# Kernel optimization log

Measured on AMD Instinct MI355X. Metric: run time of the kernel, lower is better.

Reference implementation:

```python
import jax, jax.numpy as jnp
import numpy as np


def setup_inputs() -> dict:
    key = jax.random.key(0)
    k1, k2, k3, k4, k5 = jax.random.split(key, 5)
    dim, hidden = 64, 128
    x = jax.random.normal(k1, (32, 128, 128, dim), dtype=jnp.float32)
    # torch Linear stores (out,in); we store transposed so y = x @ W + b
    W_expand = jax.random.normal(k2, (dim, hidden), dtype=jnp.float32) * (1.0 / np.sqrt(dim))
    b_expand = jax.random.normal(k3, (hidden,), dtype=jnp.float32) * 0.01
    W_restore = jax.random.normal(k4, (hidden, 1), dtype=jnp.float32) * (1.0 / np.sqrt(hidden))
    b_restore = jax.random.normal(k5, (1,), dtype=jnp.float32) * 0.01
    return {
        "x": x,
        "W_expand": W_expand,
        "b_expand": b_expand,
        "W_restore": W_restore,
        "b_restore": b_restore,
        "kernel_size": 2,
        "stride": 2,
    }


def reference(x, W_expand, b_expand, W_restore, b_restore, kernel_size, stride):
    b, r, c, d = x.shape
    sr = (r - kernel_size) // stride + 1
    sc = (c - kernel_size) // stride + 1
    s = stride  # original code slices stride x stride windows
    # gather all windows at once: (b, sr, s, sc, s, d)
    ri = (jnp.arange(sr) * stride)[:, None] + jnp.arange(s)[None, :]
    ci = (jnp.arange(sc) * stride)[:, None] + jnp.arange(s)[None, :]
    win = x[:, ri[:, :, None, None], ci[None, None, :, :], :]
    # -> (b, sr, sc, s*s, d)
    win = win.transpose(0, 1, 3, 2, 4, 5).reshape(b, sr, sc, s * s, d)
    # tiny MLP attention weights per window element
    h = jnp.tanh(jnp.einsum('bqpwd,dh->bqpwh', win, W_expand) + b_expand)
    logit = jax.nn.sigmoid(jnp.einsum('bqpwh,ho->bqpwo', h, W_restore)[..., 0] + b_restore[0])
    w = jax.nn.softmax(logit, axis=-1)  # over window elements
    out = jnp.sum(win * w[..., None], axis=3)  # (b, sr, sc, d)
    return out
```

## Files before the change

kernel.cpp:

```cpp
#include <hip/hip_runtime.h>


typedef __attribute__((ext_vector_type(8))) short short8;
typedef __attribute__((ext_vector_type(4))) float floatx4;

#define B_   32
#define R_   128
#define C_   128
#define D_   64
#define H_   128
#define NW_  (B_ * 64 * 64)
#define NGRP_ (NW_ / 4)
#define NBLK_ 1024
#define NWAVE_ (NBLK_ * 4)
#define L_   (NGRP_ / NWAVE_)

#define XSTEP_ (4L * R_ * C_ * D_)
#define OSTEP_ ((long)NWAVE_ * 4 * 64)

#define L2E_  1.4426950408889634f
#define T2L_  2.8853900817779268f

__device__ __forceinline__ unsigned short f2bf_rne(float f) {
  union { float f; unsigned int u; } v; v.f = f;
  unsigned int u = v.u;
  u += 0x7fffu + ((u >> 16) & 1u);
  return (unsigned short)(u >> 16);
}

__device__ __forceinline__ unsigned int pk_bf16(float lo, float hi) {
  unsigned int a = __builtin_bit_cast(unsigned int, lo) + 0x8000u;
  unsigned int b = __builtin_bit_cast(unsigned int, hi) + 0x8000u;
  return __builtin_amdgcn_perm(b, a, 0x07060302u);
}

template <int CTRL>
__device__ __forceinline__ float dpp_add(float x) {
  int xi = __builtin_bit_cast(int, x);
  int yi = __builtin_amdgcn_update_dpp(0, xi, CTRL, 0xf, 0xf, true);
  return x + __builtin_bit_cast(float, yi);
}
#define DPP_XOR1   0xB1
#define DPP_XOR2   0x4E
#define DPP_XOR3   0x1B
#define DPP_XOR7   0x141
#define DPP_XOR15  0x140
__device__ __forceinline__ float row_reduce16(float x) {
  x = dpp_add<DPP_XOR1>(x);
  x = dpp_add<DPP_XOR3>(x);
  x = dpp_add<DPP_XOR7>(x);
  x = dpp_add<DPP_XOR15>(x);
  return x;
}
__device__ __forceinline__ float quad_sum(float x) {
  x = dpp_add<DPP_XOR1>(x);
  x = dpp_add<DPP_XOR2>(x);
  return x;
}

__global__ void prep_kernel(const float* __restrict__ We,
                            unsigned short* __restrict__ F)
{
  int t = blockIdx.x * 256 + threadIdx.x;
  int j    = t & 7;
  int lane = (t >> 3) & 63;
  int fi   = t >> 9;
  int n  = fi >> 1, ks = fi & 1;
  int quad = lane >> 4, c = lane & 15;
  F[t] = f2bf_rne(We[(ks * 32 + quad * 8 + j) * 128 + n * 16 + c]);
}

__global__ __launch_bounds__(256, 2) void softpool_kernel(
    const float* __restrict__ x, const unsigned short* __restrict__ F,
    const float* __restrict__ be, const float* __restrict__ Wr,
    const float* __restrict__ br, float* __restrict__ out)
{
  const int lane = threadIdx.x & 63;
  const int wv   = threadIdx.x >> 6;
  const int c    = lane & 15;
  const int quad = lane >> 4;

  short8 Bf[8][2];
#pragma unroll
  for (int n = 0; n < 8; ++n)
#pragma unroll
    for (int ks = 0; ks < 2; ++ks)
      Bf[n][ks] = *(const short8*)&F[((n * 2 + ks) * 64 + lane) * 8];

  float beK[8], wr2[8], swr = 0.f;
#pragma unroll
  for (int n = 0; n < 8; ++n) {
    float w = Wr[n * 16 + c];
    beK[n] = be[n * 16 + c] * T2L_;
    wr2[n] = -2.0f * w;
    swr += w;
  }
  const float brN = -L2E_ * br[0];

  const int gw = blockIdx.x * 4 + wv;

  const int w0   = gw * 4 + (c >> 2);
  const int elem = c & 3;
  const int bb = w0 >> 12;
  const int qq = (w0 >> 6) & 63;
  const int pp = w0 & 63;
  const float* xp = x + (((bb * R_ + (qq * 2 + (elem >> 1))) * C_
                          + (pp * 2 + (elem & 1))) * D_) + quad * 8;

  const int win = c >> 2;
  float* op = out + (long)(gw * 4 + win) * 64
            + quad * 8 + ((elem & 1) << 2) + ((elem & 2) << 4);

  const int  widx = (win * 16 + elem) << 2;
  const bool oddc = (c & 1) != 0;
  const bool hi2c = (c & 2) != 0;

  floatx4 st[3][4];
#pragma unroll
  for (int s = 0; s < 2; ++s) {
    const float* p = xp + (long)s * XSTEP_;
    st[s][0] = *(const floatx4*)(p);
    st[s][1] = *(const floatx4*)(p + 4);
    st[s][2] = *(const floatx4*)(p + 32);
    st[s][3] = *(const floatx4*)(p + 36);
  }

#pragma unroll
  for (int it = 0; it < L_; ++it) {
    if (it < L_ - 2) {
      const int ps = (it + 2) % 3;
      const float* p = xp + 2 * XSTEP_;
      st[ps][0] = *(const floatx4*)(p);
      st[ps][1] = *(const floatx4*)(p + 4);
      st[ps][2] = *(const floatx4*)(p + 32);
      st[ps][3] = *(const floatx4*)(p + 36);
    }

    const int cs = it % 3;
    const floatx4 a0 = st[cs][0], a1 = st[cs][1];
    const floatx4 a2 = st[cs][2], a3 = st[cs][3];

    union { unsigned int u[4]; short8 v; } A0u, A1u;
    A0u.u[0] = pk_bf16(a0[0], a0[1]); A0u.u[1] = pk_bf16(a0[2], a0[3]);
    A0u.u[2] = pk_bf16(a1[0], a1[1]); A0u.u[3] = pk_bf16(a1[2], a1[3]);
    A1u.u[0] = pk_bf16(a2[0], a2[1]); A1u.u[1] = pk_bf16(a2[2], a2[3]);
    A1u.u[2] = pk_bf16(a3[0], a3[1]); A1u.u[3] = pk_bf16(a3[2], a3[3]);

    floatx4 acc[8];
#pragma unroll
    for (int n = 0; n < 8; ++n) {
      floatx4 z = {0.f, 0.f, 0.f, 0.f};
      z = __builtin_amdgcn_mfma_f32_16x16x32_bf16(A0u.v, Bf[n][0], z, 0, 0, 0);
      acc[n] = __builtin_amdgcn_mfma_f32_16x16x32_bf16(A1u.v, Bf[n][1], z, 0, 0, 0);
    }

    float p0 = swr, p1 = swr, p2 = swr, p3 = swr;
#pragma unroll
    for (int n = 0; n < 8; ++n) {
      float e0 = __builtin_amdgcn_exp2f(fmaf(acc[n][0], T2L_, beK[n]));
      float e1 = __builtin_amdgcn_exp2f(fmaf(acc[n][1], T2L_, beK[n]));
      float e2 = __builtin_amdgcn_exp2f(fmaf(acc[n][2], T2L_, beK[n]));
      float e3 = __builtin_amdgcn_exp2f(fmaf(acc[n][3], T2L_, beK[n]));
      p0 = fmaf(wr2[n], __builtin_amdgcn_rcpf(e0 + 1.0f), p0);
      p1 = fmaf(wr2[n], __builtin_amdgcn_rcpf(e1 + 1.0f), p1);
      p2 = fmaf(wr2[n], __builtin_amdgcn_rcpf(e2 + 1.0f), p2);
      p3 = fmaf(wr2[n], __builtin_amdgcn_rcpf(e3 + 1.0f), p3);
    }
    p0 = row_reduce16(p0);
    p1 = row_reduce16(p1);
    p2 = row_reduce16(p2);
    p3 = row_reduce16(p3);
    float l0 = __builtin_amdgcn_rcpf(1.0f + __builtin_amdgcn_exp2f(fmaf(p0, -L2E_, brN)));
    float l1 = __builtin_amdgcn_rcpf(1.0f + __builtin_amdgcn_exp2f(fmaf(p1, -L2E_, brN)));
    float l2 = __builtin_amdgcn_rcpf(1.0f + __builtin_amdgcn_exp2f(fmaf(p2, -L2E_, brN)));
    float l3 = __builtin_amdgcn_rcpf(1.0f + __builtin_amdgcn_exp2f(fmaf(p3, -L2E_, brN)));
    float s0 = __builtin_amdgcn_exp2f(l0 * L2E_);
    float s1 = __builtin_amdgcn_exp2f(l1 * L2E_);
    float s2 = __builtin_amdgcn_exp2f(l2 * L2E_);
    float s3 = __builtin_amdgcn_exp2f(l3 * L2E_);
    float inv = __builtin_amdgcn_rcpf(s0 + s1 + s2 + s3);
    float w0f = s0 * inv, w1f = s1 * inv, w2f = s2 * inv, w3f = s3 * inv;

    float wa = oddc ? w1f : w0f;
    float wb = oddc ? w3f : w2f;
    float wsel = hi2c ? wb : wa;
    float W = __builtin_bit_cast(float,
        __builtin_amdgcn_ds_bpermute(widx, __builtin_bit_cast(int, wsel)));

    floatx4 t0 = a0 * W, t1 = a1 * W, t2 = a2 * W, t3 = a3 * W;
    floatx4 o0, o1, o2, o3;
#pragma unroll
    for (int j = 0; j < 4; ++j) {
      o0[j] = quad_sum(t0[j]);
      o1[j] = quad_sum(t1[j]);
      o2[j] = quad_sum(t2[j]);
      o3[j] = quad_sum(t3[j]);
    }
    floatx4 o = hi2c ? (oddc ? o3 : o2) : (oddc ? o1 : o0);
    *(floatx4*)(op) = o;

    xp += XSTEP_;
    op += OSTEP_;
  }
}

extern "C" void kernel_launch(void* const* d_in, const int* in_sizes, int n_in,
                              void* d_out, int out_size, void* d_ws, size_t ws_size,
                              hipStream_t stream) {
  const float* x  = (const float*)d_in[0];
  const float* We = (const float*)d_in[1];
  const float* be = (const float*)d_in[2];
  const float* Wr = (const float*)d_in[3];
  const float* br = (const float*)d_in[4];
  float* out = (float*)d_out;
  unsigned short* F = (unsigned short*)d_ws;

  prep_kernel<<<32, 256, 0, stream>>>(We, F);
  softpool_kernel<<<NBLK_, 256, 0, stream>>>(x, F, be, Wr, br, out);
}
```

Measured before the change: 209.5 us.

## Raise occupancy with grid-stride loop, single-stage prefetch, and more blocks

Replaces the fully unrolled 3-stage register prefetch ring with a runtime grid-stride loop that prefetches only the next iteration. Grid size goes from 1024 to 1280 blocks and launch bounds allow 5 blocks per CU instead of 2. The aim is to hide memory latency through more resident waves rather than deep per-wave buffering, which cuts register pressure. Each wave now keeps less data in flight, and the tail handling makes the last iteration issue a redundant reload.

```diff
diff --git a/kernel.cpp b/kernel.cpp
--- a/kernel.cpp
+++ b/kernel.cpp
@@ -11,12 +11,12 @@
 #define H_   128
 #define NW_  (B_ * 64 * 64)
 #define NGRP_ (NW_ / 4)
-#define NBLK_ 1024
+#define NBLK_ 1280
 #define NWAVE_ (NBLK_ * 4)
-#define L_   (NGRP_ / NWAVE_)
-
-#define XSTEP_ (4L * R_ * C_ * D_)
-#define OSTEP_ ((long)NWAVE_ * 4 * 64)
+#define GSTRIDE_ NWAVE_
+
+#define XSTEP_ (5L * R_ * C_ * D_)
+#define OSTEP_ ((long)GSTRIDE_ * 4 * 64)
 
 #define L2E_  1.4426950408889634f
 #define T2L_  2.8853900817779268f
@@ -70,7 +70,7 @@
   F[t] = f2bf_rne(We[(ks * 32 + quad * 8 + j) * 128 + n * 16 + c]);
 }
 
-__global__ __launch_bounds__(256, 2) void softpool_kernel(
+__global__ __launch_bounds__(256, 5) void softpool_kernel(
     const float* __restrict__ x, const unsigned short* __restrict__ F,
     const float* __restrict__ be, const float* __restrict__ Wr,
     const float* __restrict__ br, float* __restrict__ out)
@@ -115,30 +115,18 @@
   const bool oddc = (c & 1) != 0;
   const bool hi2c = (c & 2) != 0;
 
-  floatx4 st[3][4];
-#pragma unroll
-  for (int s = 0; s < 2; ++s) {
-    const float* p = xp + (long)s * XSTEP_;
-    st[s][0] = *(const floatx4*)(p);
-    st[s][1] = *(const floatx4*)(p + 4);
-    st[s][2] = *(const floatx4*)(p + 32);
-    st[s][3] = *(const floatx4*)(p + 36);
-  }
-
-#pragma unroll
-  for (int it = 0; it < L_; ++it) {
-    if (it < L_ - 2) {
-      const int ps = (it + 2) % 3;
-      const float* p = xp + 2 * XSTEP_;
-      st[ps][0] = *(const floatx4*)(p);
-      st[ps][1] = *(const floatx4*)(p + 4);
-      st[ps][2] = *(const floatx4*)(p + 32);
-      st[ps][3] = *(const floatx4*)(p + 36);
-    }
-
-    const int cs = it % 3;
-    const floatx4 a0 = st[cs][0], a1 = st[cs][1];
-    const floatx4 a2 = st[cs][2], a3 = st[cs][3];
+  floatx4 a0 = *(const floatx4*)(xp);
+  floatx4 a1 = *(const floatx4*)(xp + 4);
+  floatx4 a2 = *(const floatx4*)(xp + 32);
+  floatx4 a3 = *(const floatx4*)(xp + 36);
+
+  for (int g = gw; g < NGRP_; g += GSTRIDE_) {
+    const long nd = (g + GSTRIDE_ < NGRP_) ? XSTEP_ : 0;
+    const float* xpn = xp + nd;
+    floatx4 na0 = *(const floatx4*)(xpn);
+    floatx4 na1 = *(const floatx4*)(xpn + 4);
+    floatx4 na2 = *(const floatx4*)(xpn + 32);
+    floatx4 na3 = *(const floatx4*)(xpn + 36);
 
     union { unsigned int u[4]; short8 v; } A0u, A1u;
     A0u.u[0] = pk_bf16(a0[0], a0[1]); A0u.u[1] = pk_bf16(a0[2], a0[3]);
@@ -199,8 +187,8 @@
     floatx4 o = hi2c ? (oddc ? o3 : o2) : (oddc ? o1 : o0);
     *(floatx4*)(op) = o;
 
-    xp += XSTEP_;
-    op += OSTEP_;
+    xp = xpn; op += OSTEP_;
+    a0 = na0; a1 = na1; a2 = na2; a3 = na3;
   }
 }
 
```

Result: slower. 292.1 us (+39.4%).
